# Performance work log

Measured on AMD Instinct MI355X. Metric: run time of the kernel, lower is better.

## Reference

```python
import jax, jax.numpy as jnp
import numpy as np
import math

H = 16
D_MODEL = 1024
D_K = D_MODEL // H


def setup_inputs() -> dict:
    key = jax.random.key(0)
    ks = jax.random.split(key, 12)
    B, S = 4, 2048
    inp = {
        "query": jax.random.normal(ks[0], (B, S, D_MODEL), jnp.float32),
        "key": jax.random.normal(ks[1], (B, S, D_MODEL), jnp.float32),
        "value": jax.random.normal(ks[2], (B, S, D_MODEL), jnp.float32),
        # causal mask, broadcastable over heads: [B, 1, S, S]
        "mask": jnp.broadcast_to(jnp.tril(jnp.ones((S, S), bool)), (B, 1, S, S)),
    }
    sc = 1.0 / math.sqrt(D_MODEL)
    inp["Wq"] = jax.random.normal(ks[3], (D_MODEL, D_MODEL), jnp.float32) * sc
    inp["bq"] = jnp.zeros((D_MODEL,), jnp.float32)
    inp["Wk"] = jax.random.normal(ks[4], (D_MODEL, D_MODEL), jnp.float32) * sc
    inp["bk"] = jnp.zeros((D_MODEL,), jnp.float32)
    inp["Wv"] = jax.random.normal(ks[5], (D_MODEL, D_MODEL), jnp.float32) * sc
    inp["bv"] = jnp.zeros((D_MODEL,), jnp.float32)
    inp["Wo"] = jax.random.normal(ks[6], (D_MODEL, D_MODEL), jnp.float32) * sc
    inp["bo"] = jnp.zeros((D_MODEL,), jnp.float32)
    return inp


def reference(query, key, value, mask, Wq, bq, Wk, bk, Wv, bv, Wo, bo):
    B, S, D = query.shape
    # torch nn.Linear: y = x @ W.T + b; then view(B,-1,h,d_k).transpose(1,2)
    def proj(x, W, b):
        return (x @ W.T + b).reshape(B, -1, H, D_K).transpose(0, 2, 1, 3)  # [B,h,S,d_k]

    q = proj(query, Wq, bq)
    k = proj(key, Wk, bk)
    v = proj(value, Wv, bv)

    scores = jnp.einsum("bhqd,bhkd->bhqk", q, k) / math.sqrt(D_K)
    scores = jnp.where(mask, scores, jnp.finfo(scores.dtype).min)
    p_attn = jax.nn.softmax(scores, axis=-1)  # dropout: eval mode (identity)
    x = jnp.einsum("bhqk,bhkd->bhqd", p_attn, v)
    x = x.transpose(0, 2, 1, 3).reshape(B, -1, H * D_K)
    return x @ Wo.T + bo
```

## Files before the change

### kernel.cpp

```cpp
#include <hip/hip_runtime.h>
#include <hip/hip_bf16.h>

typedef unsigned short u16;
typedef unsigned int u32;
typedef __attribute__((ext_vector_type(8))) short short8;
typedef __attribute__((ext_vector_type(4))) short short4v;
typedef __attribute__((ext_vector_type(4))) float f32x4;
typedef __attribute__((ext_vector_type(4))) float float4_t;

#define DIM 1024
#define NH  16
#define DKK 64
#define SEQ 2048
#define NB  4
#define SM_SCALE 0.1803368801111244f

__device__ __forceinline__ u16 f2bf(float f) {
    __bf16 h = (__bf16)f;
    return __builtin_bit_cast(u16, h);
}

__device__ __forceinline__ f32x4 mfma_bf16(short8 a, short8 b, f32x4 c) {
    return __builtin_amdgcn_mfma_f32_16x16x32_bf16(a, b, c, 0, 0, 0);
}

__device__ __forceinline__ short8 pack8(float4_t a, float4_t b) {
    short8 v;
    v[0] = (short)f2bf(a[0]); v[1] = (short)f2bf(a[1]);
    v[2] = (short)f2bf(a[2]); v[3] = (short)f2bf(a[3]);
    v[4] = (short)f2bf(b[0]); v[5] = (short)f2bf(b[1]);
    v[6] = (short)f2bf(b[2]); v[7] = (short)f2bf(b[3]);
    return v;
}

typedef const __attribute__((address_space(1))) u32* gas1_t;
typedef __attribute__((address_space(3))) u32* las3_t;
__device__ __forceinline__ void g2l16(const void* g, void* l) {
    __builtin_amdgcn_global_load_lds((gas1_t)g, (las3_t)l, 16, 0, 0);
}

__device__ __forceinline__ float max16(const f32x4* s) {
    const float a = fmaxf(fmaxf(s[0][0], s[0][1]), fmaxf(s[0][2], s[0][3]));
    const float b = fmaxf(fmaxf(s[1][0], s[1][1]), fmaxf(s[1][2], s[1][3]));
    const float c = fmaxf(fmaxf(s[2][0], s[2][1]), fmaxf(s[2][2], s[2][3]));
    const float d = fmaxf(fmaxf(s[3][0], s[3][1]), fmaxf(s[3][2], s[3][3]));
    return fmaxf(fmaxf(a, b), fmaxf(c, d));
}

__global__ __launch_bounds__(256) void conv8(const float* __restrict__ src,
                                             u16* __restrict__ dst) {
    const int i = (blockIdx.x * 256 + threadIdx.x) * 8;
    const float4_t a = *(const float4_t*)(src + i);
    const float4_t b = *(const float4_t*)(src + i + 4);
    *(short8*)(dst + i) = pack8(a, b);
}

__global__ __launch_bounds__(256) void conv8w(const float* __restrict__ w0,
                                              const float* __restrict__ w1,
                                              const float* __restrict__ w2,
                                              const float* __restrict__ w3,
                                              u16* __restrict__ dst) {
    const int t = blockIdx.y;
    const float* s = t == 0 ? w0 : t == 1 ? w1 : t == 2 ? w2 : w3;
    const int i = (blockIdx.x * 256 + threadIdx.x) * 8;
    const float4_t a = *(const float4_t*)(s + i);
    const float4_t b = *(const float4_t*)(s + i + 4);
    *(short8*)(dst + (size_t)t * DIM * DIM + i) = pack8(a, b);
}

template<int MODE>
__global__ __launch_bounds__(256)
void gemmb(const u16* __restrict__ A, const u16* __restrict__ Bw,
           const float* __restrict__ bias, float scale,
           u16* __restrict__ Cbf, float* __restrict__ Cf)
{
    __shared__ __align__(16) u16 As[128][32];
    __shared__ __align__(16) u16 Bs[128][32];
    const int tid  = threadIdx.x;
    const int lane = tid & 63;
    const int w    = tid >> 6;
    const int wr   = w >> 1, wc = w & 1;
    const int m0   = blockIdx.y * 128;
    const int n0   = blockIdx.x * 128;
    const int lm   = lane & 15, lg = lane >> 4;
    const int srow = lane >> 2;
    const int scol = (lane & 3) * 8;

    f32x4 acc[4][4];
#pragma unroll
    for (int i = 0; i < 4; ++i)
#pragma unroll
        for (int j = 0; j < 4; ++j) acc[i][j] = (f32x4){0.f, 0.f, 0.f, 0.f};

    for (int k0 = 0; k0 < DIM; k0 += 32) {
        __syncthreads();
#pragma unroll
        for (int i = 0; i < 2; ++i) {
            g2l16(A  + (size_t)(m0 + w * 32 + i * 16 + srow) * DIM + k0 + scol,
                  &As[w * 32 + i * 16][0]);
            g2l16(Bw + (size_t)(n0 + w * 32 + i * 16 + srow) * DIM + k0 + scol,
                  &Bs[w * 32 + i * 16][0]);
        }
        __syncthreads();

        short8 af[4], bfr[4];
#pragma unroll
        for (int t = 0; t < 4; ++t) {
            af[t]  = *(const short8*)&As[wr * 64 + t * 16 + lm][lg * 8];
            bfr[t] = *(const short8*)&Bs[wc * 64 + t * 16 + lm][lg * 8];
        }
#pragma unroll
        for (int mt = 0; mt < 4; ++mt)
#pragma unroll
            for (int nt = 0; nt < 4; ++nt)
                acc[mt][nt] = mfma_bf16(af[mt], bfr[nt], acc[mt][nt]);
    }

#pragma unroll
    for (int mt = 0; mt < 4; ++mt)
#pragma unroll
        for (int nt = 0; nt < 4; ++nt)
#pragma unroll
            for (int r = 0; r < 4; ++r) {
                const int m = m0 + wr * 64 + mt * 16 + lg * 4 + r;
                const int n = n0 + wc * 64 + nt * 16 + lm;
                if (MODE == 0) {
                    const float val = (acc[mt][nt][r] + bias[n]) * scale;
                    const int b = m >> 11, s = m & 2047;
                    const int h = n >> 6,  dk = n & 63;
                    Cbf[(((size_t)b * NH + h) * SEQ + s) * DKK + dk] = f2bf(val);
                } else if (MODE == 1) {
                    Cf[(size_t)m * DIM + n] = acc[mt][nt][r] + bias[n];
                } else {
                    const float val = acc[mt][nt][r] + bias[m];
                    const int h = m >> 6, dk = m & 63;
                    const int b = n >> 11, s = n & 2047;
                    Cbf[(((size_t)b * NH + h) * DKK + dk) * SEQ + s] = f2bf(val);
                }
            }
}

__global__ __launch_bounds__(256, 2)
void attn3(const u16* __restrict__ Q, const u16* __restrict__ K,
           const u16* __restrict__ Vt, u16* __restrict__ O)
{
    __shared__ __align__(16) u16 Ks[64][72];
    __shared__ __align__(16) u16 Vs[64][72];
    __shared__ __align__(16) u16 Ps[4][32][72];

    const int tid  = threadIdx.x;
    const int lane = tid & 63;
    const int w    = tid >> 6;
    const int lm   = lane & 15, lg = lane >> 4;
    const int Lr   = blockIdx.y * gridDim.x + blockIdx.x;
    const int work = (Lr & 7) * 128 + (Lr >> 3);
    const int pb   = work & 15;
    const int bh   = work >> 4;
    const int Abase = pb * 64;
    const int Bbase = SEQ - 64 - Abase;
    const int qA = Abase + 16 * w;
    const int qB = Bbase + 16 * w;
    const u16* Qp = Q  + (size_t)bh * SEQ * DKK;
    const u16* Kp = K  + (size_t)bh * SEQ * DKK;
    const u16* Vp = Vt + (size_t)bh * DKK * SEQ;

    short8 qa[2][2];
#pragma unroll
    for (int kh = 0; kh < 2; ++kh) {
        qa[0][kh] = *(const short8*)(Qp + (size_t)(qA + lm) * DKK + kh * 32 + lg * 8);
        qa[1][kh] = *(const short8*)(Qp + (size_t)(qB + lm) * DKK + kh * 32 + lg * 8);
    }

    float m_q[2] = {-INFINITY, -INFINITY};
    float l_q[2] = {0.f, 0.f};
    f32x4 o[2][4];
#pragma unroll
    for (int qt = 0; qt < 2; ++qt)
#pragma unroll
        for (int dt = 0; dt < 4; ++dt) o[qt][dt] = (f32x4){0.f, 0.f, 0.f, 0.f};

    const f32x4 zero = (f32x4){0.f, 0.f, 0.f, 0.f};
    const int srow = tid >> 3;
    const int soct = (tid & 7) * 8;
    const int kv_end = Bbase + 64;

    short8 rk0 = *(const short8*)(Kp + (size_t)srow * DKK + soct);
    short8 rk1 = *(const short8*)(Kp + (size_t)(srow + 32) * DKK + soct);
    short8 rv0 = *(const short8*)(Vp + (size_t)srow * SEQ + soct);
    short8 rv1 = *(const short8*)(Vp + (size_t)(srow + 32) * SEQ + soct);

    for (int kv0 = 0; kv0 < kv_end; kv0 += 64) {
        __syncthreads();
        *(short8*)&Ks[srow][soct]      = rk0;
        *(short8*)&Ks[srow + 32][soct] = rk1;
        *(short8*)&Vs[srow][soct]      = rv0;
        *(short8*)&Vs[srow + 32][soct] = rv1;
        const int nkv = kv0 + 64;
        if (nkv < kv_end) {
            rk0 = *(const short8*)(Kp + (size_t)(nkv + srow) * DKK + soct);
            rk1 = *(const short8*)(Kp + (size_t)(nkv + srow + 32) * DKK + soct);
            rv0 = *(const short8*)(Vp + (size_t)srow * SEQ + nkv + soct);
            rv1 = *(const short8*)(Vp + (size_t)(srow + 32) * SEQ + nkv + soct);
        }
        __syncthreads();

        const bool actA = kv0 < qA + 16;
        const bool msk[2] = { kv0 + 63 > qA, kv0 + 63 > qB };
        const bool act[2] = { actA, true };
        const int  qb[2]  = { qA, qB };

        f32x4 s[2][4];
#pragma unroll
        for (int kvt = 0; kvt < 4; ++kvt) {
            const short8 kb0 = *(const short8*)&Ks[kvt * 16 + lm][lg * 8];
            const short8 kb1 = *(const short8*)&Ks[kvt * 16 + lm][32 + lg * 8];
            s[1][kvt] = mfma_bf16(kb1, qa[1][1], mfma_bf16(kb0, qa[1][0], zero));
            if (actA)
                s[0][kvt] = mfma_bf16(kb1, qa[0][1], mfma_bf16(kb0, qa[0][0], zero));
        }

        float mx[2] = {-INFINITY, -INFINITY};
#pragma unroll
        for (int qt = 0; qt < 2; ++qt) {
            if (!act[qt]) continue;
            if (msk[qt]) {
                const int q = qb[qt] + lm;
#pragma unroll
                for (int kvt = 0; kvt < 4; ++kvt)
#pragma unroll
                    for (int r = 0; r < 4; ++r) {
                        const int kv = kv0 + kvt * 16 + lg * 4 + r;
                        if (kv > q) s[qt][kvt][r] = -INFINITY;
                    }
            }
            float vmax = max16(s[qt]);
            vmax = fmaxf(vmax, __shfl_xor(vmax, 16));
            vmax = fmaxf(vmax, __shfl_xor(vmax, 32));
            mx[qt] = vmax;
        }

        const bool small = (!actA || mx[0] <= m_q[0] + 8.f) && (mx[1] <= m_q[1] + 8.f);
        if (__all(small)) {
#pragma unroll
            for (int qt = 0; qt < 2; ++qt) {
                if (!act[qt]) continue;
                float part[4];
#pragma unroll
                for (int kvt = 0; kvt < 4; ++kvt) {
                    short4v pk;
                    f32x4 p;
#pragma unroll
                    for (int r = 0; r < 4; ++r) {
                        p[r] = __builtin_exp2f(s[qt][kvt][r] - m_q[qt]);
                        pk[r] = (short)f2bf(p[r]);
                    }
                    part[kvt] = (p[0] + p[1]) + (p[2] + p[3]);
                    *(short4v*)&Ps[w][qt * 16 + lm][kvt * 16 + lg * 4] = pk;
                }
                l_q[qt] += (part[0] + part[1]) + (part[2] + part[3]);
            }
        } else {
#pragma unroll
            for (int qt = 0; qt < 2; ++qt) {
                if (!act[qt]) continue;
                const float mnew = fmaxf(m_q[qt], mx[qt]);
                const float alpha = __builtin_exp2f(m_q[qt] - mnew);
                m_q[qt] = mnew;
                float part[4];
#pragma unroll
                for (int kvt = 0; kvt < 4; ++kvt) {
                    short4v pk;
                    f32x4 p;
#pragma unroll
                    for (int r = 0; r < 4; ++r) {
                        p[r] = __builtin_exp2f(s[qt][kvt][r] - mnew);
                        pk[r] = (short)f2bf(p[r]);
                    }
                    part[kvt] = (p[0] + p[1]) + (p[2] + p[3]);
                    *(short4v*)&Ps[w][qt * 16 + lm][kvt * 16 + lg * 4] = pk;
                }
                l_q[qt] = l_q[qt] * alpha + (part[0] + part[1]) + (part[2] + part[3]);
#pragma unroll
                for (int r = 0; r < 4; ++r) {
                    const float ar = __shfl(alpha, lg * 4 + r);
#pragma unroll
                    for (int dt = 0; dt < 4; ++dt) o[qt][dt][r] *= ar;
                }
            }
        }
        asm volatile("s_waitcnt lgkmcnt(0)" ::: "memory");

        short8 pa[2][2], vbt[4][2];
#pragma unroll
        for (int qt = 0; qt < 2; ++qt)
            if (act[qt]) {
                pa[qt][0] = *(const short8*)&Ps[w][qt * 16 + lm][lg * 8];
                pa[qt][1] = *(const short8*)&Ps[w][qt * 16 + lm][32 + lg * 8];
            }
#pragma unroll
        for (int dt = 0; dt < 4; ++dt) {
            vbt[dt][0] = *(const short8*)&Vs[dt * 16 + lm][lg * 8];
            vbt[dt][1] = *(const short8*)&Vs[dt * 16 + lm][32 + lg * 8];
        }
#pragma unroll
        for (int dt = 0; dt < 4; ++dt)
#pragma unroll
            for (int qt = 0; qt < 2; ++qt) {
                if (!act[qt]) continue;
                o[qt][dt] = mfma_bf16(pa[qt][1], vbt[dt][1],
                                      mfma_bf16(pa[qt][0], vbt[dt][0], o[qt][dt]));
            }
    }

    const int b = bh >> 4, h = bh & 15;
#pragma unroll
    for (int qt = 0; qt < 2; ++qt) {
        float lf = l_q[qt];
        lf += __shfl_xor(lf, 16);
        lf += __shfl_xor(lf, 32);
        const int qbase = qt ? qB : qA;
#pragma unroll
        for (int r = 0; r < 4; ++r) {
            const float li = 1.f / __shfl(lf, lg * 4 + r);
            const int srw = qbase + lg * 4 + r;
#pragma unroll
            for (int dt = 0; dt < 4; ++dt)
                O[(((size_t)b * SEQ + srw) * NH + h) * DKK + dt * 16 + lm] =
                    f2bf(o[qt][dt][r] * li);
        }
    }
}

extern "C" void kernel_launch(void* const* d_in, const int* in_sizes, int n_in,
                              void* d_out, int out_size, void* d_ws, size_t ws_size,
                              hipStream_t stream)
{
    const float* query = (const float*)d_in[0];
    const float* key   = (const float*)d_in[1];
    const float* value = (const float*)d_in[2];
    const float* Wq = (const float*)d_in[4];
    const float* bq = (const float*)d_in[5];
    const float* Wk = (const float*)d_in[6];
    const float* bk = (const float*)d_in[7];
    const float* Wv = (const float*)d_in[8];
    const float* bv = (const float*)d_in[9];
    const float* Wo = (const float*)d_in[10];
    const float* bo = (const float*)d_in[11];
    float* out = (float*)d_out;

    const size_t HD = (size_t)NB * NH * SEQ * DKK;
    const size_t WSZ = (size_t)DIM * DIM;
    u16* qws  = (u16*)d_ws;
    u16* kws  = qws + HD;
    u16* vtws = kws + HD;
    u16* ows  = vtws + HD;
    u16* wbf  = ows + HD;
    u16* cvt  = ows;

    dim3 gg(DIM / 128, (NB * SEQ) / 128);
    dim3 gv((NB * SEQ) / 128, DIM / 128);
    const int ca = (int)(HD / 2048);
    conv8w<<<dim3(WSZ / 2048, 4), 256, 0, stream>>>(Wq, Wk, Wv, Wo, wbf);

    conv8<<<ca, 256, 0, stream>>>(query, cvt);
    gemmb<0><<<gg, 256, 0, stream>>>(cvt, wbf, bq, SM_SCALE, qws, nullptr);
    conv8<<<ca, 256, 0, stream>>>(key, cvt);
    gemmb<0><<<gg, 256, 0, stream>>>(cvt, wbf + WSZ, bk, 1.f, kws, nullptr);
    conv8<<<ca, 256, 0, stream>>>(value, cvt);
    gemmb<2><<<gv, 256, 0, stream>>>(wbf + 2 * WSZ, cvt, bv, 1.f, vtws, nullptr);

    attn3<<<dim3(16, NB * NH), 256, 0, stream>>>(qws, kws, vtws, ows);
    gemmb<1><<<gg, 256, 0, stream>>>(ows, wbf + 3 * WSZ, bo, 1.f, nullptr, out);
}
```

Measured before the change: 245.9 us.

## Software-pipeline attention: overlap previous tile's PV MFMA with current QK and softmax

Restructures the attention loop so the P·V matmul for the previous KV tile runs right after the current tile's QK^T MFMAs, with V double-buffered in shared memory and a tail step after the loop. The aim is to hide softmax exp/VALU latency behind matrix work and remove the explicit lgkmcnt wait. It also raises wave priority around the MFMA section and drops the occupancy hint of 2 from launch_bounds. This adds LDS usage and keeps the P tile live across iterations, which may raise register pressure and lower occupancy.

```diff
diff --git a/kernel.cpp b/kernel.cpp
--- a/kernel.cpp
+++ b/kernel.cpp
@@ -140,12 +140,12 @@
             }
 }
 
-__global__ __launch_bounds__(256, 2)
-void attn3(const u16* __restrict__ Q, const u16* __restrict__ K,
+__global__ __launch_bounds__(256)
+void attn4(const u16* __restrict__ Q, const u16* __restrict__ K,
            const u16* __restrict__ Vt, u16* __restrict__ O)
 {
     __shared__ __align__(16) u16 Ks[64][72];
-    __shared__ __align__(16) u16 Vs[64][72];
+    __shared__ __align__(16) u16 Vs[2][64][72];
     __shared__ __align__(16) u16 Ps[4][32][72];
 
     const int tid  = threadIdx.x;
@@ -189,12 +189,15 @@
     short8 rv0 = *(const short8*)(Vp + (size_t)srow * SEQ + soct);
     short8 rv1 = *(const short8*)(Vp + (size_t)(srow + 32) * SEQ + soct);
 
+    bool pA = false;
+
     for (int kv0 = 0; kv0 < kv_end; kv0 += 64) {
+        const int cur = (kv0 >> 6) & 1;
         __syncthreads();
-        *(short8*)&Ks[srow][soct]      = rk0;
-        *(short8*)&Ks[srow + 32][soct] = rk1;
-        *(short8*)&Vs[srow][soct]      = rv0;
-        *(short8*)&Vs[srow + 32][soct] = rv1;
+        *(short8*)&Ks[srow][soct]          = rk0;
+        *(short8*)&Ks[srow + 32][soct]     = rk1;
+        *(short8*)&Vs[cur][srow][soct]      = rv0;
+        *(short8*)&Vs[cur][srow + 32][soct] = rv1;
         const int nkv = kv0 + 64;
         if (nkv < kv_end) {
             rk0 = *(const short8*)(Kp + (size_t)(nkv + srow) * DKK + soct);
@@ -206,9 +209,9 @@
 
         const bool actA = kv0 < qA + 16;
         const bool msk[2] = { kv0 + 63 > qA, kv0 + 63 > qB };
-        const bool act[2] = { actA, true };
         const int  qb[2]  = { qA, qB };
 
+        __builtin_amdgcn_s_setprio(1);
         f32x4 s[2][4];
 #pragma unroll
         for (int kvt = 0; kvt < 4; ++kvt) {
@@ -219,10 +222,34 @@
                 s[0][kvt] = mfma_bf16(kb1, qa[0][1], mfma_bf16(kb0, qa[0][0], zero));
         }
 
+        if (kv0 > 0) {
+            short8 pa[2][2], vbt[4][2];
+#pragma unroll
+            for (int qt = 0; qt < 2; ++qt)
+                if (qt || pA) {
+                    pa[qt][0] = *(const short8*)&Ps[w][qt * 16 + lm][lg * 8];
+                    pa[qt][1] = *(const short8*)&Ps[w][qt * 16 + lm][32 + lg * 8];
+                }
+#pragma unroll
+            for (int dt = 0; dt < 4; ++dt) {
+                vbt[dt][0] = *(const short8*)&Vs[cur ^ 1][dt * 16 + lm][lg * 8];
+                vbt[dt][1] = *(const short8*)&Vs[cur ^ 1][dt * 16 + lm][32 + lg * 8];
+            }
+#pragma unroll
+            for (int dt = 0; dt < 4; ++dt)
+#pragma unroll
+                for (int qt = 0; qt < 2; ++qt) {
+                    if (!qt && !pA) continue;
+                    o[qt][dt] = mfma_bf16(pa[qt][1], vbt[dt][1],
+                                          mfma_bf16(pa[qt][0], vbt[dt][0], o[qt][dt]));
+                }
+        }
+        __builtin_amdgcn_s_setprio(0);
+
         float mx[2] = {-INFINITY, -INFINITY};
 #pragma unroll
         for (int qt = 0; qt < 2; ++qt) {
-            if (!act[qt]) continue;
+            if (!qt && !actA) continue;
             if (msk[qt]) {
                 const int q = qb[qt] + lm;
 #pragma unroll
@@ -243,7 +270,7 @@
         if (__all(small)) {
 #pragma unroll
             for (int qt = 0; qt < 2; ++qt) {
-                if (!act[qt]) continue;
+                if (!qt && !actA) continue;
                 float part[4];
 #pragma unroll
                 for (int kvt = 0; kvt < 4; ++kvt) {
@@ -262,7 +289,7 @@
         } else {
 #pragma unroll
             for (int qt = 0; qt < 2; ++qt) {
-                if (!act[qt]) continue;
+                if (!qt && !actA) continue;
                 const float mnew = fmaxf(m_q[qt], mx[qt]);
                 const float alpha = __builtin_exp2f(m_q[qt] - mnew);
                 m_q[qt] = mnew;
@@ -288,25 +315,28 @@
                 }
             }
         }
-        asm volatile("s_waitcnt lgkmcnt(0)" ::: "memory");
-
+        pA = actA;
+    }
+
+    {
+        const int cur = ((kv_end - 64) >> 6) & 1;
         short8 pa[2][2], vbt[4][2];
 #pragma unroll
         for (int qt = 0; qt < 2; ++qt)
-            if (act[qt]) {
+            if (qt || pA) {
                 pa[qt][0] = *(const short8*)&Ps[w][qt * 16 + lm][lg * 8];
                 pa[qt][1] = *(const short8*)&Ps[w][qt * 16 + lm][32 + lg * 8];
             }
 #pragma unroll
         for (int dt = 0; dt < 4; ++dt) {
-            vbt[dt][0] = *(const short8*)&Vs[dt * 16 + lm][lg * 8];
-            vbt[dt][1] = *(const short8*)&Vs[dt * 16 + lm][32 + lg * 8];
+            vbt[dt][0] = *(const short8*)&Vs[cur][dt * 16 + lm][lg * 8];
+            vbt[dt][1] = *(const short8*)&Vs[cur][dt * 16 + lm][32 + lg * 8];
         }
 #pragma unroll
         for (int dt = 0; dt < 4; ++dt)
 #pragma unroll
             for (int qt = 0; qt < 2; ++qt) {
-                if (!act[qt]) continue;
+                if (!qt && !pA) continue;
                 o[qt][dt] = mfma_bf16(pa[qt][1], vbt[dt][1],
                                       mfma_bf16(pa[qt][0], vbt[dt][0], o[qt][dt]));
             }
@@ -369,6 +399,6 @@
     conv8<<<ca, 256, 0, stream>>>(value, cvt);
     gemmb<2><<<gv, 256, 0, stream>>>(wbf + 2 * WSZ, cvt, bv, 1.f, vtws, nullptr);
 
-    attn3<<<dim3(16, NB * NH), 256, 0, stream>>>(qws, kws, vtws, ows);
+    attn4<<<dim3(16, NB * NH), 256, 0, stream>>>(qws, kws, vtws, ows);
     gemmb<1><<<gg, 256, 0, stream>>>(ows, wbf + 3 * WSZ, bo, 1.f, nullptr, out);
 }
```

Measured after the change: 256.7 us. 1.04x slower.
